# Optimization experiments

Measured on AMD Instinct MI355X. Metric: run time of the kernel, lower is better.

Reference implementation:

```python
import jax, jax.numpy as jnp
import numpy as np

B, CIN, H, W = 16, 256, 56, 56
D, HEADS, KS, PAD, STRIDE, M = 256, 8, 3, 1, 1, 4
K = KS * KS
N = D // HEADS
# relative_indices: sum of window coords, flattened row-major, values in [0, 2*KS-2]
REL = (np.arange(KS)[:, None] + np.arange(KS)[None, :]).reshape(-1)


def setup_inputs() -> dict:
    key = jax.random.key(0)
    ks = jax.random.split(key, 7)
    return {
        "x": jax.random.normal(ks[0], (B, CIN, H, W), jnp.float32),
        "q": jax.random.normal(ks[1], (B, D, 1), jnp.float32),
        "Wk": jax.random.normal(ks[2], (D, CIN), jnp.float32) * 0.05,
        "Wv": jax.random.normal(ks[3], (D, CIN), jnp.float32) * 0.05,
        "pos_emb": jax.random.normal(ks[4], (1, 2 * KS - 1), jnp.float32),
        "Wlin": jax.random.normal(ks[5], (1, M), jnp.float32),
        "Wproj": jax.random.normal(ks[6], (D, D), jnp.float32) * 0.05,
    }


def _unfold(t):
    # torch nn.Unfold: (B,C,H,W) -> (B, C*K, L); patches feature dim ordered (C, kh, kw)
    p = jax.lax.conv_general_dilated_patches(
        t, (KS, KS), (STRIDE, STRIDE), [(PAD, PAD), (PAD, PAD)])
    b, _, ho, wo = p.shape
    return p.reshape(b, -1, ho * wo), ho, wo


def reference(x, q, Wk, Wv, pos_emb, Wlin, Wproj):
    b = x.shape[0]
    k = jnp.einsum('oc,bchw->bohw', Wk, x)  # 1x1 conv, no bias
    v = jnp.einsum('oc,bchw->bohw', Wv, x)
    ku, ho, wo = _unfold(k)
    vu, _, _ = _unfold(v)
    L = ho * wo
    ku = ku.reshape(b, HEADS, N, K, L)  # (b, h, n, k, l)
    vu = vu.reshape(b, HEADS, N, K, L)
    qh = q.reshape(b, HEADS, N)  # learned per-batch query, d=1 squeezed
    attn = jnp.einsum('bhn,bhnkl->bhlk', qh, ku)  # (b,h,l,K)
    attn = attn + pos_emb[0, REL]  # relative position bias, shape (K,)
    attn = jax.nn.softmax(attn, axis=-1)
    # repeat d(=1) -> m identical rows then Linear(m,1,no bias): equals scale by sum(Wlin)
    attn = attn * jnp.sum(Wlin)
    out = jnp.einsum('bhlk,bhnkl->bhnl', attn, vu)  # (b,h,n,l)
    out = out.reshape(b, D, ho, wo)  # fold with kernel 1 == reshape
    return jnp.einsum('oc,bchw->bohw', Wproj, out)  # 1x1 proj conv
```

## Files before the change

### kernel.cpp

```cpp
#include <hip/hip_runtime.h>

#define B_     16
#define D_     256
#define HEADS_ 8
#define N_     32
#define H_     56
#define W_     56
#define L_     3136
#define BL_    (B_ * L_)

typedef short short8 __attribute__((ext_vector_type(8)));
typedef float f32x4  __attribute__((ext_vector_type(4)));

__device__ __forceinline__ unsigned short f2bf(float f) {
    union { float f; unsigned u; } c; c.f = f;
    unsigned u = c.u;
    u += 0x7fffu + ((u >> 16) & 1u);
    return (unsigned short)(u >> 16);
}

#define GL2L(g, l) __builtin_amdgcn_global_load_lds( \
    (const __attribute__((address_space(1))) void*)(g), \
    (__attribute__((address_space(3))) void*)(l), 16, 0, 0)

__global__ __launch_bounds__(256) void convert_w_kernel(
    const float* __restrict__ Wv, const float* __restrict__ Wproj,
    const float* __restrict__ Wk, const float* __restrict__ q,
    unsigned short* __restrict__ Wvb, unsigned short* __restrict__ Wpb,
    float* __restrict__ qt)
{
    if (blockIdx.y < 2) {
        const float* src   = (blockIdx.y == 0) ? Wv  : Wproj;
        unsigned short* dst = (blockIdx.y == 0) ? Wvb : Wpb;
        const int i = (blockIdx.x * 256 + threadIdx.x) * 4;
        float4 v = *(const float4*)(src + i);
        uint2 o;
        o.x = (unsigned)f2bf(v.x) | ((unsigned)f2bf(v.y) << 16);
        o.y = (unsigned)f2bf(v.z) | ((unsigned)f2bf(v.w) << 16);
        *(uint2*)(dst + i) = o;
    } else {
        const int b  = blockIdx.x >> 2;
        const int h0 = (blockIdx.x & 3) * 2;
        const int c  = threadIdx.x;
#pragma unroll
        for (int hh = 0; hh < 2; ++hh) {
            const int h = h0 + hh;
            const float* qb = q  + b * D_ + h * N_;
            const float* wr = Wk + (size_t)(h * N_) * D_ + c;
            float acc = 0.f;
#pragma unroll 8
            for (int n = 0; n < N_; ++n)
                acc = fmaf(qb[n], wr[(size_t)n * D_], acc);
            qt[((size_t)b * HEADS_ + h) * D_ + c] = acc;
        }
    }
}

__global__ __launch_bounds__(256) void transpose_x_kernel(
    const float* __restrict__ x, unsigned short* __restrict__ Xt)
{
    __shared__ float tile[64][65];
    const int bb = blockIdx.z;
    const int c0 = blockIdx.y * 64;
    const int l0 = blockIdx.x * 64;
    const int t  = threadIdx.x;
    const int g4 = (t & 15) * 4;
    const int rr = t >> 4;

    const float* xb = x + ((size_t)bb * D_ + c0) * L_ + l0;
#pragma unroll
    for (int i = 0; i < 4; ++i) {
        const int c = rr + i * 16;
        float4 v = *(const float4*)(xb + (size_t)c * L_ + g4);
        *(float4*)&tile[c][g4] = v;
    }
    __syncthreads();
    unsigned short* Xb = Xt + ((size_t)bb * L_ + l0) * D_ + c0;
#pragma unroll
    for (int i = 0; i < 4; ++i) {
        const int l = rr + i * 16;
        uint2 o;
        o.x = (unsigned)f2bf(tile[g4 + 0][l]) | ((unsigned)f2bf(tile[g4 + 1][l]) << 16);
        o.y = (unsigned)f2bf(tile[g4 + 2][l]) | ((unsigned)f2bf(tile[g4 + 3][l]) << 16);
        *(uint2*)(Xb + (size_t)l * D_ + g4) = o;
    }
}

__global__ __launch_bounds__(256) void s_kernel(
    const float* __restrict__ x, const float* __restrict__ qt,
    float* __restrict__ S)
{
    __shared__ float  qs[HEADS_ * D_];
    __shared__ float4 red[4][HEADS_ * 64];

    const int bb = blockIdx.y;
    const int l0 = blockIdx.x * 256;
    const int t  = threadIdx.x;
    const int sl = t & 63;
    const int cq = t >> 6;

    {
        const float4* s4 = (const float4*)(qt + (size_t)bb * HEADS_ * D_);
        ((float4*)qs)[t]       = s4[t];
        ((float4*)qs)[t + 256] = s4[t + 256];
    }
    __syncthreads();

    float4 sacc[8];
#pragma unroll
    for (int h = 0; h < 8; ++h) sacc[h] = (float4){0.f, 0.f, 0.f, 0.f};

    const int l = l0 + sl * 4;
    if (l < L_) {
        const float* xb = x + (size_t)bb * D_ * L_ + l;
#pragma unroll 4
        for (int c = cq * 64; c < cq * 64 + 64; ++c) {
            const float4 xv = *(const float4*)(xb + (size_t)c * L_);
#pragma unroll
            for (int h = 0; h < 8; ++h) {
                const float qv = qs[h * D_ + c];
                sacc[h].x = fmaf(qv, xv.x, sacc[h].x);
                sacc[h].y = fmaf(qv, xv.y, sacc[h].y);
                sacc[h].z = fmaf(qv, xv.z, sacc[h].z);
                sacc[h].w = fmaf(qv, xv.w, sacc[h].w);
            }
        }
    }

#pragma unroll
    for (int h = 0; h < 8; ++h) red[cq][h * 64 + sl] = sacc[h];
    __syncthreads();

    for (int j = t; j < 512; j += 256) {
        const int h = j >> 6, s = j & 63;
        const int lw = l0 + s * 4;
        if (lw < L_) {
            const float4 a = red[0][h * 64 + s];
            const float4 b = red[1][h * 64 + s];
            const float4 c = red[2][h * 64 + s];
            const float4 d = red[3][h * 64 + s];
            float4 o;
            o.x = a.x + b.x + c.x + d.x;
            o.y = a.y + b.y + c.y + d.y;
            o.z = a.z + b.z + c.z + d.z;
            o.w = a.w + b.w + c.w + d.w;
            *(float4*)(S + ((size_t)bb * HEADS_ + h) * L_ + lw) = o;
        }
    }
}

__global__ __launch_bounds__(256) void gemm_v_mfma(
    const unsigned short* __restrict__ Xt, const unsigned short* __restrict__ Wvb,
    unsigned short* __restrict__ Vo)
{
    __shared__ unsigned short As[2][128 * 32];
    __shared__ unsigned short Bs[2][128 * 32];

    const int t = threadIdx.x;
    const int w = t >> 6, lane = t & 63, col = lane & 15, quad = lane >> 4;
    const int wr = w >> 1, wc = w & 1;
    const int n0 = blockIdx.x * 128;
    const int d0 = blockIdx.y * 128;
    const int srow = t >> 2;
    const int skc  = (t & 3) * 8;

    const unsigned short* Ag = Wvb + (size_t)(d0 + srow) * D_ + skc;
    const unsigned short* Bg = Xt + (size_t)(n0 + srow) * D_ + skc;

    f32x4 acc[4][4];
#pragma unroll
    for (int m = 0; m < 4; ++m)
#pragma unroll
        for (int n = 0; n < 4; ++n) acc[m][n] = (f32x4){0.f, 0.f, 0.f, 0.f};

    {
        char* An = (char*)&As[0][0] + w * 1024;
        char* Bn = (char*)&Bs[0][0] + w * 1024;
        GL2L(Ag, An);            GL2L(Ag + 64 * D_, An + 4096);
        GL2L(Bg, Bn);            GL2L(Bg + 64 * D_, Bn + 4096);
    }
    __syncthreads();

#pragma unroll
    for (int kt = 0; kt < 8; ++kt) {
        const int cur = kt & 1;
        if (kt < 7) {
            const int c1 = (kt + 1) * 32;
            char* An = (char*)&As[cur ^ 1][0] + w * 1024;
            char* Bn = (char*)&Bs[cur ^ 1][0] + w * 1024;
            GL2L(Ag + c1, An);           GL2L(Ag + 64 * D_ + c1, An + 4096);
            GL2L(Bg + c1, Bn);           GL2L(Bg + 64 * D_ + c1, Bn + 4096);
        }
        const unsigned short* Ab = &As[cur][0];
        const unsigned short* Bb = &Bs[cur][0];
        short8 af[4], bf[4];
#pragma unroll
        for (int m = 0; m < 4; ++m)
            af[m] = *(const short8*)(Ab + (wr * 64 + m * 16 + col) * 32 + quad * 8);
#pragma unroll
        for (int n = 0; n < 4; ++n)
            bf[n] = *(const short8*)(Bb + (wc * 64 + n * 16 + col) * 32 + quad * 8);
#pragma unroll
        for (int m = 0; m < 4; ++m)
#pragma unroll
            for (int n = 0; n < 4; ++n)
                acc[m][n] = __builtin_amdgcn_mfma_f32_16x16x32_bf16(af[m], bf[n], acc[m][n], 0, 0, 0);
        __syncthreads();
    }

#pragma unroll
    for (int n = 0; n < 4; ++n) {
        const unsigned flat = n0 + wc * 64 + n * 16 + col;
        const unsigned bq = flat / L_;
        const unsigned lq = flat - bq * L_;
#pragma unroll
        for (int m = 0; m < 4; ++m) {
            const int d  = d0 + wr * 64 + m * 16 + quad * 4;
            const int h  = d >> 5;
            const int dn = d & 31;
            unsigned short ob[4];
#pragma unroll
            for (int r = 0; r < 4; ++r) ob[r] = f2bf(acc[m][n][r]);
            *(uint2*)(Vo + ((size_t)(bq * HEADS_ + h) * L_ + lq) * N_ + dn) =
                *(const uint2*)ob;
        }
    }
}

__global__ __launch_bounds__(256) void attend_kernel(
    const float* __restrict__ S, const unsigned short* __restrict__ Vo,
    const float* __restrict__ pos_emb, const float* __restrict__ Wlin,
    unsigned short* __restrict__ Om)
{
    __shared__ __align__(16) unsigned short Vs[600 * 32];
    __shared__ float Ss[10][58];

    const int band = blockIdx.x;
    const int bh   = blockIdx.y;
    const int y0   = band * 8;
    const int t    = threadIdx.x;

    const float* Sb = S + (size_t)bh * L_;
    for (int wi = t; wi < 580; wi += 256) {
        const int row = wi / 58, c = wi - row * 58;
        const int gr = y0 - 1 + row, gc = c - 1;
        float v = 0.f;
        if (gr >= 0 && gr < H_ && gc >= 0 && gc < W_)
            v = Sb[gr * W_ + gc];
        Ss[row][c] = v;
    }

    const unsigned short* Vbase = Vo + (size_t)bh * L_ * N_;
    for (int wi = t; wi < 2400; wi += 256) {
        const int p = wi >> 2, i = wi & 3;
        const int row = p / 60, cc = p - row * 60;
        const int gr = y0 - 1 + row, gc = cc - 1;
        uint4 v = make_uint4(0u, 0u, 0u, 0u);
        if (gr >= 0 && gr < H_ && gc >= 0 && gc < W_)
            v = *(const uint4*)(Vbase + (size_t)(gr * W_ + gc) * N_ + i * 8);
        const int sfc = wi ^ (p & 7);
        *(uint4*)(Vs + sfc * 8) = v;
    }
    __syncthreads();

    const float scale = Wlin[0] + Wlin[1] + Wlin[2] + Wlin[3];
    const float pe0 = pos_emb[0], pe1 = pos_emb[1], pe2 = pos_emb[2];
    const float pe3 = pos_emb[3], pe4 = pos_emb[4];
    const float bias[9] = {pe0, pe1, pe2, pe1, pe2, pe3, pe2, pe3, pe4};

    for (int idx = t; idx < 448; idx += 256) {
        const int yl = idx / 56, xx = idx - yl * 56;
        const int lr = yl + 1, lc = xx + 1;

        float lg[9], m = -1e30f;
#pragma unroll
        for (int dy = 0; dy < 3; ++dy)
#pragma unroll
            for (int dx = 0; dx < 3; ++dx) {
                const int k = dy * 3 + dx;
                lg[k] = Ss[lr - 1 + dy][lc - 1 + dx] + bias[k];
                m = fmaxf(m, lg[k]);
            }
        float ssum = 0.f;
#pragma unroll
        for (int k = 0; k < 9; ++k) { lg[k] = __expf(lg[k] - m); ssum += lg[k]; }
        const float inv = scale / ssum;

        float om[32];
#pragma unroll
        for (int i = 0; i < 32; ++i) om[i] = 0.f;

#pragma unroll
        for (int dy = 0; dy < 3; ++dy)
#pragma unroll
            for (int dx = 0; dx < 3; ++dx) {
                const float wk = lg[dy * 3 + dx] * inv;
                const int pos  = (lr - 1 + dy) * 60 + (lc - 1 + dx);
                const int base = pos * 4;
                const int msk  = pos & 7;
#pragma unroll
                for (int i = 0; i < 4; ++i) {
                    const int sfc = (base + i) ^ msk;
                    const uint4 v = *(const uint4*)(Vs + sfc * 8);
                    const unsigned* u = (const unsigned*)&v;
#pragma unroll
                    for (int j = 0; j < 4; ++j) {
                        union { unsigned uu; float f; } lo, hi;
                        lo.uu = u[j] << 16;
                        hi.uu = u[j] & 0xffff0000u;
                        om[i * 8 + 2 * j]     = fmaf(wk, lo.f, om[i * 8 + 2 * j]);
                        om[i * 8 + 2 * j + 1] = fmaf(wk, hi.f, om[i * 8 + 2 * j + 1]);
                    }
                }
            }

        unsigned short ob[32];
#pragma unroll
        for (int i = 0; i < 32; ++i) ob[i] = f2bf(om[i]);
        const int l = (y0 + yl) * W_ + xx;
        uint4* dst = (uint4*)(Om + ((size_t)bh * L_ + l) * N_);
        const uint4* sb = (const uint4*)ob;
#pragma unroll
        for (int i = 0; i < 4; ++i) dst[i] = sb[i];
    }
}

__global__ __launch_bounds__(256) void gemm_proj_mfma(
    const unsigned short* __restrict__ Om, const unsigned short* __restrict__ Wpb,
    float* __restrict__ Out)
{
    __shared__ unsigned short As[2][128 * 32];
    __shared__ unsigned short Bs[2][128 * 32];

    const int t = threadIdx.x;
    const int w = t >> 6, lane = t & 63, col = lane & 15, quad = lane >> 4;
    const int wr = w >> 1, wc = w & 1;
    const int n0 = blockIdx.x * 128;
    const int d0 = blockIdx.y * 128;
    const int srow = t >> 2;
    const int skc  = (t & 3) * 8;

    const unsigned short* Ag = Wpb + (size_t)(d0 + srow) * D_ + skc;
    const int f0 = n0 + srow;
    const unsigned b0q = (unsigned)f0 / L_, l0q = (unsigned)f0 - b0q * L_;
    const int f1 = f0 + 64;
    const unsigned b1q = (unsigned)f1 / L_, l1q = (unsigned)f1 - b1q * L_;
    const unsigned short* Bg0 = Om + ((size_t)(b0q * HEADS_) * L_ + l0q) * N_ + skc;
    const unsigned short* Bg1 = Om + ((size_t)(b1q * HEADS_) * L_ + l1q) * N_ + skc;
    const size_t kstride = (size_t)L_ * N_;

    f32x4 acc[4][4];
#pragma unroll
    for (int m = 0; m < 4; ++m)
#pragma unroll
        for (int n = 0; n < 4; ++n) acc[m][n] = (f32x4){0.f, 0.f, 0.f, 0.f};

    {
        char* An = (char*)&As[0][0] + w * 1024;
        char* Bn = (char*)&Bs[0][0] + w * 1024;
        GL2L(Ag, An);            GL2L(Ag + 64 * D_, An + 4096);
        GL2L(Bg0, Bn);           GL2L(Bg1, Bn + 4096);
    }
    __syncthreads();

#pragma unroll
    for (int kt = 0; kt < 8; ++kt) {
        const int cur = kt & 1;
        if (kt < 7) {
            const int c1 = (kt + 1) * 32;
            char* An = (char*)&As[cur ^ 1][0] + w * 1024;
            char* Bn = (char*)&Bs[cur ^ 1][0] + w * 1024;
            GL2L(Ag + c1, An);                     GL2L(Ag + 64 * D_ + c1, An + 4096);
            GL2L(Bg0 + (kt + 1) * kstride, Bn);    GL2L(Bg1 + (kt + 1) * kstride, Bn + 4096);
        }
        const unsigned short* Ab = &As[cur][0];
        const unsigned short* Bb = &Bs[cur][0];
        short8 af[4], bf[4];
#pragma unroll
        for (int m = 0; m < 4; ++m)
            af[m] = *(const short8*)(Ab + (wr * 64 + m * 16 + col) * 32 + quad * 8);
#pragma unroll
        for (int n = 0; n < 4; ++n)
            bf[n] = *(const short8*)(Bb + (wc * 64 + n * 16 + col) * 32 + quad * 8);
#pragma unroll
        for (int m = 0; m < 4; ++m)
#pragma unroll
            for (int n = 0; n < 4; ++n)
                acc[m][n] = __builtin_amdgcn_mfma_f32_16x16x32_bf16(af[m], bf[n], acc[m][n], 0, 0, 0);
        __syncthreads();
    }

#pragma unroll
    for (int n = 0; n < 4; ++n) {
        const unsigned flat = n0 + wc * 64 + n * 16 + col;
        const unsigned bq = flat / L_;
        const unsigned lq = flat - bq * L_;
        float* oout = Out + (size_t)bq * D_ * L_ + lq;
#pragma unroll
        for (int m = 0; m < 4; ++m) {
            const int dbase = d0 + wr * 64 + m * 16 + quad * 4;
#pragma unroll
            for (int r = 0; r < 4; ++r)
                oout[(size_t)(dbase + r) * L_] = acc[m][n][r];
        }
    }
}

extern "C" void kernel_launch(void* const* d_in, const int* in_sizes, int n_in,
                              void* d_out, int out_size, void* d_ws, size_t ws_size,
                              hipStream_t stream)
{
    const float* x       = (const float*)d_in[0];
    const float* q       = (const float*)d_in[1];
    const float* Wk      = (const float*)d_in[2];
    const float* Wv      = (const float*)d_in[3];
    const float* pos_emb = (const float*)d_in[4];
    const float* Wlin    = (const float*)d_in[5];
    const float* Wproj   = (const float*)d_in[6];
    float* out = (float*)d_out;

    const size_t planeE = (size_t)B_ * D_ * L_;
    unsigned short* Xt  = (unsigned short*)d_ws;
    unsigned short* Vo  = Xt + planeE;
    unsigned short* Om  = Vo + planeE;
    unsigned short* Wvb = Om + planeE;
    unsigned short* Wpb = Wvb + D_ * D_;
    float*          S   = (float*)(Wpb + D_ * D_);
    float*          qt  = S + (size_t)B_ * HEADS_ * L_;

    convert_w_kernel<<<dim3(64, 3), 256, 0, stream>>>(Wv, Wproj, Wk, q, Wvb, Wpb, qt);
    transpose_x_kernel<<<dim3(L_ / 64, D_ / 64, B_), 256, 0, stream>>>(x, Xt);
    s_kernel<<<dim3((L_ + 255) / 256, B_), 256, 0, stream>>>(x, qt, S);
    gemm_v_mfma<<<dim3(BL_ / 128, 2), 256, 0, stream>>>(Xt, Wvb, Vo);
    attend_kernel<<<dim3(7, B_ * HEADS_), 256, 0, stream>>>(S, Vo, pos_emb, Wlin, Om);
    gemm_proj_mfma<<<dim3(BL_ / 128, 2), 256, 0, stream>>>(Om, Wpb, out);
}
```

Measured before the change: 177.2 us.

## Fuse x transpose/bf16 conversion into V GEMM, load B operand directly

Removes the separate transpose_x kernel and its bf16 workspace. The V GEMM now reads fp32 x directly from global memory into registers, converts to bf16 in-register and feeds MFMA, with the whole 128x256 weight tile staged once in padded LDS. The projection GEMM likewise loads its B operand straight from global instead of through double-buffered LDS, and the S kernel is re-split into 128-column blocks with 8 channel groups for more parallelism. This saves a full write and read of the transposed activation, but the V GEMM's global loads are strided per channel, and both GEMMs lose software prefetch and latency hiding.

```diff
diff --git a/kernel.cpp b/kernel.cpp
--- a/kernel.cpp
+++ b/kernel.cpp
@@ -8,6 +8,7 @@
 #define W_     56
 #define L_     3136
 #define BL_    (B_ * L_)
+#define LDA_A  264
 
 typedef short short8 __attribute__((ext_vector_type(8)));
 typedef float f32x4  __attribute__((ext_vector_type(4)));
@@ -18,10 +19,6 @@
     u += 0x7fffu + ((u >> 16) & 1u);
     return (unsigned short)(u >> 16);
 }
-
-#define GL2L(g, l) __builtin_amdgcn_global_load_lds( \
-    (const __attribute__((address_space(1))) void*)(g), \
-    (__attribute__((address_space(3))) void*)(l), 16, 0, 0)
 
 __global__ __launch_bounds__(256) void convert_w_kernel(
     const float* __restrict__ Wv, const float* __restrict__ Wproj,
@@ -56,48 +53,18 @@
     }
 }
 
-__global__ __launch_bounds__(256) void transpose_x_kernel(
-    const float* __restrict__ x, unsigned short* __restrict__ Xt)
-{
-    __shared__ float tile[64][65];
-    const int bb = blockIdx.z;
-    const int c0 = blockIdx.y * 64;
-    const int l0 = blockIdx.x * 64;
-    const int t  = threadIdx.x;
-    const int g4 = (t & 15) * 4;
-    const int rr = t >> 4;
-
-    const float* xb = x + ((size_t)bb * D_ + c0) * L_ + l0;
-#pragma unroll
-    for (int i = 0; i < 4; ++i) {
-        const int c = rr + i * 16;
-        float4 v = *(const float4*)(xb + (size_t)c * L_ + g4);
-        *(float4*)&tile[c][g4] = v;
-    }
-    __syncthreads();
-    unsigned short* Xb = Xt + ((size_t)bb * L_ + l0) * D_ + c0;
-#pragma unroll
-    for (int i = 0; i < 4; ++i) {
-        const int l = rr + i * 16;
-        uint2 o;
-        o.x = (unsigned)f2bf(tile[g4 + 0][l]) | ((unsigned)f2bf(tile[g4 + 1][l]) << 16);
-        o.y = (unsigned)f2bf(tile[g4 + 2][l]) | ((unsigned)f2bf(tile[g4 + 3][l]) << 16);
-        *(uint2*)(Xb + (size_t)l * D_ + g4) = o;
-    }
-}
-
 __global__ __launch_bounds__(256) void s_kernel(
     const float* __restrict__ x, const float* __restrict__ qt,
     float* __restrict__ S)
 {
     __shared__ float  qs[HEADS_ * D_];
-    __shared__ float4 red[4][HEADS_ * 64];
+    __shared__ float4 red[8][HEADS_][32];
 
     const int bb = blockIdx.y;
-    const int l0 = blockIdx.x * 256;
+    const int l0 = blockIdx.x * 128;
     const int t  = threadIdx.x;
-    const int sl = t & 63;
-    const int cq = t >> 6;
+    const int lg = t & 31;
+    const int cg = t >> 5;
 
     {
         const float4* s4 = (const float4*)(qt + (size_t)bb * HEADS_ * D_);
@@ -110,11 +77,11 @@
 #pragma unroll
     for (int h = 0; h < 8; ++h) sacc[h] = (float4){0.f, 0.f, 0.f, 0.f};
 
-    const int l = l0 + sl * 4;
+    const int l = l0 + lg * 4;
     if (l < L_) {
         const float* xb = x + (size_t)bb * D_ * L_ + l;
 #pragma unroll 4
-        for (int c = cq * 64; c < cq * 64 + 64; ++c) {
+        for (int c = cg * 32; c < cg * 32 + 32; ++c) {
             const float4 xv = *(const float4*)(xb + (size_t)c * L_);
 #pragma unroll
             for (int h = 0; h < 8; ++h) {
@@ -128,44 +95,54 @@
     }
 
 #pragma unroll
-    for (int h = 0; h < 8; ++h) red[cq][h * 64 + sl] = sacc[h];
-    __syncthreads();
-
-    for (int j = t; j < 512; j += 256) {
-        const int h = j >> 6, s = j & 63;
-        const int lw = l0 + s * 4;
+    for (int h = 0; h < 8; ++h) red[cg][h][lg] = sacc[h];
+    __syncthreads();
+
+    {
+        const int h  = t >> 5;
+        const int l2 = t & 31;
+        const int lw = l0 + l2 * 4;
         if (lw < L_) {
-            const float4 a = red[0][h * 64 + s];
-            const float4 b = red[1][h * 64 + s];
-            const float4 c = red[2][h * 64 + s];
-            const float4 d = red[3][h * 64 + s];
-            float4 o;
-            o.x = a.x + b.x + c.x + d.x;
-            o.y = a.y + b.y + c.y + d.y;
-            o.z = a.z + b.z + c.z + d.z;
-            o.w = a.w + b.w + c.w + d.w;
+            float4 o = (float4){0.f, 0.f, 0.f, 0.f};
+#pragma unroll
+            for (int g = 0; g < 8; ++g) {
+                const float4 v = red[g][h][l2];
+                o.x += v.x; o.y += v.y; o.z += v.z; o.w += v.w;
+            }
             *(float4*)(S + ((size_t)bb * HEADS_ + h) * L_ + lw) = o;
         }
     }
 }
 
 __global__ __launch_bounds__(256) void gemm_v_mfma(
-    const unsigned short* __restrict__ Xt, const unsigned short* __restrict__ Wvb,
+    const float* __restrict__ x, const unsigned short* __restrict__ Wvb,
     unsigned short* __restrict__ Vo)
 {
-    __shared__ unsigned short As[2][128 * 32];
-    __shared__ unsigned short Bs[2][128 * 32];
+    __shared__ __align__(16) unsigned short As[128 * LDA_A];
 
     const int t = threadIdx.x;
     const int w = t >> 6, lane = t & 63, col = lane & 15, quad = lane >> 4;
     const int wr = w >> 1, wc = w & 1;
     const int n0 = blockIdx.x * 128;
     const int d0 = blockIdx.y * 128;
-    const int srow = t >> 2;
-    const int skc  = (t & 3) * 8;
-
-    const unsigned short* Ag = Wvb + (size_t)(d0 + srow) * D_ + skc;
-    const unsigned short* Bg = Xt + (size_t)(n0 + srow) * D_ + skc;
+
+#pragma unroll
+    for (int i = 0; i < 16; ++i) {
+        const int u   = t + i * 256;
+        const int row = u >> 5;
+        const int cu  = (u & 31) * 8;
+        uint4 v = *(const uint4*)(Wvb + (size_t)(d0 + row) * D_ + cu);
+        *(uint4*)&As[row * LDA_A + cu] = v;
+    }
+
+    const float* xb[4];
+#pragma unroll
+    for (int n = 0; n < 4; ++n) {
+        const unsigned flat = n0 + wc * 64 + n * 16 + col;
+        const unsigned bq = flat / L_;
+        const unsigned lq = flat - bq * L_;
+        xb[n] = x + ((size_t)bq * D_ + quad * 8) * L_ + lq;
+    }
 
     f32x4 acc[4][4];
 #pragma unroll
@@ -173,39 +150,33 @@
 #pragma unroll
         for (int n = 0; n < 4; ++n) acc[m][n] = (f32x4){0.f, 0.f, 0.f, 0.f};
 
-    {
-        char* An = (char*)&As[0][0] + w * 1024;
-        char* Bn = (char*)&Bs[0][0] + w * 1024;
-        GL2L(Ag, An);            GL2L(Ag + 64 * D_, An + 4096);
-        GL2L(Bg, Bn);            GL2L(Bg + 64 * D_, Bn + 4096);
-    }
     __syncthreads();
 
 #pragma unroll
     for (int kt = 0; kt < 8; ++kt) {
-        const int cur = kt & 1;
-        if (kt < 7) {
-            const int c1 = (kt + 1) * 32;
-            char* An = (char*)&As[cur ^ 1][0] + w * 1024;
-            char* Bn = (char*)&Bs[cur ^ 1][0] + w * 1024;
-            GL2L(Ag + c1, An);           GL2L(Ag + 64 * D_ + c1, An + 4096);
-            GL2L(Bg + c1, Bn);           GL2L(Bg + 64 * D_ + c1, Bn + 4096);
-        }
-        const unsigned short* Ab = &As[cur][0];
-        const unsigned short* Bb = &Bs[cur][0];
-        short8 af[4], bf[4];
+        short8 bf[4];
+#pragma unroll
+        for (int n = 0; n < 4; ++n) {
+            float f[8];
+#pragma unroll
+            for (int j = 0; j < 8; ++j)
+                f[j] = xb[n][(size_t)(kt * 32 + j) * L_];
+            union { unsigned u[4]; short8 s; } pk;
+#pragma unroll
+            for (int p = 0; p < 4; ++p)
+                asm("v_cvt_pk_bf16_f32 %0, %1, %2"
+                    : "=v"(pk.u[p]) : "v"(f[2 * p]), "v"(f[2 * p + 1]));
+            bf[n] = pk.s;
+        }
+        short8 af[4];
 #pragma unroll
         for (int m = 0; m < 4; ++m)
-            af[m] = *(const short8*)(Ab + (wr * 64 + m * 16 + col) * 32 + quad * 8);
-#pragma unroll
-        for (int n = 0; n < 4; ++n)
-            bf[n] = *(const short8*)(Bb + (wc * 64 + n * 16 + col) * 32 + quad * 8);
+            af[m] = *(const short8*)&As[(wr * 64 + m * 16 + col) * LDA_A + kt * 32 + quad * 8];
 #pragma unroll
         for (int m = 0; m < 4; ++m)
 #pragma unroll
             for (int n = 0; n < 4; ++n)
                 acc[m][n] = __builtin_amdgcn_mfma_f32_16x16x32_bf16(af[m], bf[n], acc[m][n], 0, 0, 0);
-        __syncthreads();
     }
 
 #pragma unroll
@@ -329,24 +300,31 @@
     const unsigned short* __restrict__ Om, const unsigned short* __restrict__ Wpb,
     float* __restrict__ Out)
 {
-    __shared__ unsigned short As[2][128 * 32];
-    __shared__ unsigned short Bs[2][128 * 32];
+    __shared__ __align__(16) unsigned short As[128 * LDA_A];
 
     const int t = threadIdx.x;
     const int w = t >> 6, lane = t & 63, col = lane & 15, quad = lane >> 4;
     const int wr = w >> 1, wc = w & 1;
     const int n0 = blockIdx.x * 128;
     const int d0 = blockIdx.y * 128;
-    const int srow = t >> 2;
-    const int skc  = (t & 3) * 8;
-
-    const unsigned short* Ag = Wpb + (size_t)(d0 + srow) * D_ + skc;
-    const int f0 = n0 + srow;
-    const unsigned b0q = (unsigned)f0 / L_, l0q = (unsigned)f0 - b0q * L_;
-    const int f1 = f0 + 64;
-    const unsigned b1q = (unsigned)f1 / L_, l1q = (unsigned)f1 - b1q * L_;
-    const unsigned short* Bg0 = Om + ((size_t)(b0q * HEADS_) * L_ + l0q) * N_ + skc;
-    const unsigned short* Bg1 = Om + ((size_t)(b1q * HEADS_) * L_ + l1q) * N_ + skc;
+
+#pragma unroll
+    for (int i = 0; i < 16; ++i) {
+        const int u   = t + i * 256;
+        const int row = u >> 5;
+        const int cu  = (u & 31) * 8;
+        uint4 v = *(const uint4*)(Wpb + (size_t)(d0 + row) * D_ + cu);
+        *(uint4*)&As[row * LDA_A + cu] = v;
+    }
+
+    const unsigned short* ob[4];
+#pragma unroll
+    for (int n = 0; n < 4; ++n) {
+        const unsigned flat = n0 + wc * 64 + n * 16 + col;
+        const unsigned bq = flat / L_;
+        const unsigned lq = flat - bq * L_;
+        ob[n] = Om + ((size_t)(bq * HEADS_) * L_ + lq) * N_ + quad * 8;
+    }
     const size_t kstride = (size_t)L_ * N_;
 
     f32x4 acc[4][4];
@@ -355,39 +333,22 @@
 #pragma unroll
         for (int n = 0; n < 4; ++n) acc[m][n] = (f32x4){0.f, 0.f, 0.f, 0.f};
 
-    {
-        char* An = (char*)&As[0][0] + w * 1024;
-        char* Bn = (char*)&Bs[0][0] + w * 1024;
-        GL2L(Ag, An);            GL2L(Ag + 64 * D_, An + 4096);
-        GL2L(Bg0, Bn);           GL2L(Bg1, Bn + 4096);
-    }
     __syncthreads();
 
 #pragma unroll
     for (int kt = 0; kt < 8; ++kt) {
-        const int cur = kt & 1;
-        if (kt < 7) {
-            const int c1 = (kt + 1) * 32;
-            char* An = (char*)&As[cur ^ 1][0] + w * 1024;
-            char* Bn = (char*)&Bs[cur ^ 1][0] + w * 1024;
-            GL2L(Ag + c1, An);                     GL2L(Ag + 64 * D_ + c1, An + 4096);
-            GL2L(Bg0 + (kt + 1) * kstride, Bn);    GL2L(Bg1 + (kt + 1) * kstride, Bn + 4096);
-        }
-        const unsigned short* Ab = &As[cur][0];
-        const unsigned short* Bb = &Bs[cur][0];
-        short8 af[4], bf[4];
+        short8 bf[4], af[4];
+#pragma unroll
+        for (int n = 0; n < 4; ++n)
+            bf[n] = *(const short8*)(ob[n] + (size_t)kt * kstride);
 #pragma unroll
         for (int m = 0; m < 4; ++m)
-            af[m] = *(const short8*)(Ab + (wr * 64 + m * 16 + col) * 32 + quad * 8);
-#pragma unroll
-        for (int n = 0; n < 4; ++n)
-            bf[n] = *(const short8*)(Bb + (wc * 64 + n * 16 + col) * 32 + quad * 8);
+            af[m] = *(const short8*)&As[(wr * 64 + m * 16 + col) * LDA_A + kt * 32 + quad * 8];
 #pragma unroll
         for (int m = 0; m < 4; ++m)
 #pragma unroll
             for (int n = 0; n < 4; ++n)
                 acc[m][n] = __builtin_amdgcn_mfma_f32_16x16x32_bf16(af[m], bf[n], acc[m][n], 0, 0, 0);
-        __syncthreads();
     }
 
 #pragma unroll
@@ -420,8 +381,7 @@
     float* out = (float*)d_out;
 
     const size_t planeE = (size_t)B_ * D_ * L_;
-    unsigned short* Xt  = (unsigned short*)d_ws;
-    unsigned short* Vo  = Xt + planeE;
+    unsigned short* Vo  = (unsigned short*)d_ws;
     unsigned short* Om  = Vo + planeE;
     unsigned short* Wvb = Om + planeE;
     unsigned short* Wpb = Wvb + D_ * D_;
@@ -429,9 +389,8 @@
     float*          qt  = S + (size_t)B_ * HEADS_ * L_;
 
     convert_w_kernel<<<dim3(64, 3), 256, 0, stream>>>(Wv, Wproj, Wk, q, Wvb, Wpb, qt);
-    transpose_x_kernel<<<dim3(L_ / 64, D_ / 64, B_), 256, 0, stream>>>(x, Xt);
-    s_kernel<<<dim3((L_ + 255) / 256, B_), 256, 0, stream>>>(x, qt, S);
-    gemm_v_mfma<<<dim3(BL_ / 128, 2), 256, 0, stream>>>(Xt, Wvb, Vo);
+    s_kernel<<<dim3((L_ + 127) / 128, B_), 256, 0, stream>>>(x, qt, S);
+    gemm_v_mfma<<<dim3(BL_ / 128, 2), 256, 0, stream>>>(x, Wvb, Vo);
     attend_kernel<<<dim3(7, B_ * HEADS_), 256, 0, stream>>>(S, Vo, pos_emb, Wlin, Om);
     gemm_proj_mfma<<<dim3(BL_ / 128, 2), 256, 0, stream>>>(Om, Wpb, out);
 }
```

Measured after the change: 174.6 us. No clear change (-1.5%).
